# Optimization experiments

Hardware: AMD Instinct MI355X
Metric: run time of the kernel (lower is better)

The kernel has to match this reference:

```python
import jax, jax.numpy as jnp
import numpy as np

D_STATE = 16
D_CONV = 4
EXPAND = 2
GROUPS = 8
EPS = 1e-5


def _layernorm(x, w, b):
    m = x.mean(-1, keepdims=True)
    v = x.var(-1, keepdims=True)
    return (x - m) * jax.lax.rsqrt(v + EPS) * w + b


def _groupnorm(x, w, b):
    B, C = x.shape[:2]
    sp = x.shape[2:]
    xg = x.reshape(B, GROUPS, C // GROUPS, -1)
    m = xg.mean(axis=(2, 3), keepdims=True)
    v = xg.var(axis=(2, 3), keepdims=True)
    xg = (xg - m) * jax.lax.rsqrt(v + EPS)
    x = xg.reshape((B, C) + sp)
    shp = (1, C) + (1,) * len(sp)
    return x * w.reshape(shp) + b.reshape(shp)


def _mamba(xn, in_w, conv_w, conv_b, xp_w, dt_w, dt_b, A_log, Dp, out_w):
    # xn: [B, L, C]
    B, L, C = xn.shape
    di = in_w.shape[0] // 2
    rank = dt_w.shape[1]
    N = D_STATE
    xz = xn @ in_w.T                              # [B, L, 2*di]
    xi, z = xz[..., :di], xz[..., di:]
    # causal depthwise conv1d along L (pad left d_conv-1, truncate to L)
    xc = jnp.moveaxis(xi, 1, 2)                   # [B, di, L]
    xpd = jnp.pad(xc, ((0, 0), (0, 0), (D_CONV - 1, 0)))
    conv = conv_b[None, :, None]
    for k in range(D_CONV):
        conv = conv + conv_w[None, :, k, None] * xpd[:, :, k:k + L]
    u = jnp.moveaxis(jax.nn.silu(conv), 1, 2)     # [B, L, di]
    dbl = u @ xp_w.T                              # [B, L, rank+2N]
    dt = dbl[..., :rank]
    Bm = dbl[..., rank:rank + N]
    Cm = dbl[..., rank + N:]
    delta = jax.nn.softplus(dt @ dt_w.T + dt_b)   # [B, L, di]
    A = -jnp.exp(A_log)                           # [di, N]
    dA = jnp.exp(delta[..., None] * A)            # [B, L, di, N]
    dBu = delta[..., None] * Bm[:, :, None, :] * u[..., None]

    def comb(e1, e2):
        a1, b1 = e1
        a2, b2 = e2
        return a1 * a2, a2 * b1 + b2

    _, h = jax.lax.associative_scan(comb, (dA, dBu), axis=1)  # h_t = dA_t*h_{t-1} + dBu_t
    y = jnp.einsum('bldn,bln->bld', h, Cm) + u * Dp
    y = y * jax.nn.silu(z)
    return y @ out_w.T


def _mamba_layer(x, p):
    B, C = x.shape[:2]
    img = x.shape[2:]
    L = int(np.prod(img))
    xf = jnp.moveaxis(x.reshape(B, C, L), 1, 2)   # [B, L, C]
    xn = _layernorm(xf, p['ln_w'], p['ln_b'])
    xm = _mamba(xn, p['in_w'], p['conv_w'], p['conv_b'], p['xp_w'],
                p['dt_w'], p['dt_b'], p['A_log'], p['Dp'], p['out_w'])
    xm = xm + p['skip'] * xf
    xm = _layernorm(xm, p['ln_w'], p['ln_b'])     # same norm params reused, as in source
    y = xm @ p['proj_w'].T + p['proj_b']
    return jnp.moveaxis(y, 1, 2).reshape((B, C) + img)


def setup_inputs() -> dict:
    key = jax.random.key(0)
    B, C = 2, 48
    img = (16, 32, 32)
    di = EXPAND * C
    rank = -(-C // 16)
    ks = iter(jax.random.split(key, 64))

    def nrm(shape, scale):
        return jax.random.normal(next(ks), shape, jnp.float32) * scale

    inp = {'x': jax.random.normal(next(ks), (B, C) + img, jnp.float32)}
    inp['gn1_w'] = jnp.ones(C); inp['gn1_b'] = jnp.zeros(C)
    inp['gn2_w'] = jnp.ones(C); inp['gn2_b'] = jnp.zeros(C)
    for i in (1, 2):
        inp[f'ln{i}_w'] = jnp.ones(C); inp[f'ln{i}_b'] = jnp.zeros(C)
        inp[f'in_w{i}'] = nrm((2 * di, C), C ** -0.5)
        inp[f'conv_w{i}'] = nrm((di, D_CONV), D_CONV ** -0.5)
        inp[f'conv_b{i}'] = jnp.zeros(di)
        inp[f'xp_w{i}'] = nrm((rank + 2 * D_STATE, di), di ** -0.5)
        inp[f'dt_w{i}'] = nrm((di, rank), rank ** -0.5)
        inp[f'dt_b{i}'] = nrm((di,), 0.1) - 4.0  # softplus -> small positive dt
        inp[f'A_log{i}'] = jnp.log(jnp.tile(jnp.arange(1, D_STATE + 1, dtype=jnp.float32), (di, 1)))
        inp[f'D{i}'] = jnp.ones(di)
        inp[f'out_w{i}'] = nrm((C, di), di ** -0.5)
        inp[f'proj_w{i}'] = nrm((C, C), C ** -0.5)
        inp[f'proj_b{i}'] = jnp.zeros(C)
        inp[f'skip{i}'] = jnp.ones(1)
    return inp


def reference(x, gn1_w, gn1_b, gn2_w, gn2_b,
              ln1_w, ln1_b, in_w1, conv_w1, conv_b1, xp_w1, dt_w1, dt_b1, A_log1, D1, out_w1, proj_w1, proj_b1, skip1,
              ln2_w, ln2_b, in_w2, conv_w2, conv_b2, xp_w2, dt_w2, dt_b2, A_log2, D2, out_w2, proj_w2, proj_b2, skip2):
    p1 = dict(ln_w=ln1_w, ln_b=ln1_b, in_w=in_w1, conv_w=conv_w1, conv_b=conv_b1, xp_w=xp_w1,
              dt_w=dt_w1, dt_b=dt_b1, A_log=A_log1, Dp=D1, out_w=out_w1, proj_w=proj_w1,
              proj_b=proj_b1, skip=skip1)
    p2 = dict(ln_w=ln2_w, ln_b=ln2_b, in_w=in_w2, conv_w=conv_w2, conv_b=conv_b2, xp_w=xp_w2,
              dt_w=dt_w2, dt_b=dt_b2, A_log=A_log2, Dp=D2, out_w=out_w2, proj_w=proj_w2,
              proj_b=proj_b2, skip=skip2)
    identity = x
    h = jax.nn.relu(_groupnorm(x, gn1_w, gn1_b))
    h = _mamba_layer(h, p1)
    h = jax.nn.relu(_groupnorm(h, gn2_w, gn2_b))
    h = _mamba_layer(h, p2)
    return h + identity
```

## Files before the change

kernel.cpp:

```cpp
#include <hip/hip_runtime.h>
#include <hip/hip_bf16.h>

#define LCH   48
#define DI    96
#define LSEQ  16384
#define NB    2
#define NPOS  (NB*LSEQ)
#define NSTATE 16
#define CPG   6
#define EPS   1e-5f
#define NC    128
#define CL    128
#define NCHAIN (NB*DI*NSTATE)
#define TS    32
#define TSS   36

typedef __hip_bfloat16 bf16;

__device__ __forceinline__ float LDW(const void* p, size_t i, bool f32){
    return f32 ? ((const float*)p)[i] : __bfloat162float(((const bf16*)p)[i]);
}

__device__ __forceinline__ float bf2f(unsigned short h){
    union { unsigned int i; float f; } u; u.i = ((unsigned int)h) << 16; return u.f;
}

__device__ __forceinline__ float4 LDW4(const void* p, size_t i4, bool f32){
    if (f32) return ((const float4*)p)[i4];
    ushort4 v = ((const ushort4*)p)[i4];
    return make_float4(bf2f(v.x), bf2f(v.y), bf2f(v.z), bf2f(v.w));
}

__device__ __forceinline__ float row16_sum(float p){
    union { float f; int i; } u, v;
    u.f = p; v.i = __builtin_amdgcn_mov_dpp(u.i, 0x111, 0xf, 0xf, true); p += v.f;
    u.f = p; v.i = __builtin_amdgcn_mov_dpp(u.i, 0x112, 0xf, 0xf, true); p += v.f;
    u.f = p; v.i = __builtin_amdgcn_mov_dpp(u.i, 0x114, 0xf, 0xf, true); p += v.f;
    u.f = p; v.i = __builtin_amdgcn_mov_dpp(u.i, 0x118, 0xf, 0xf, true); p += v.f;
    return p;
}

__global__ void k_flag(const void* gnw, int* flag, float* __restrict__ acc1, float* __restrict__ acc2){
    int t = threadIdx.x;
    if (t == 0){
        const unsigned short* g = (const unsigned short*)gnw;
        flag[0] = (g[0] == 0x3F80) ? 0 : 1;
    }
    if (t < 32){ acc1[t] = 0.f; acc2[t] = 0.f; }
}

__global__ void k_gnpart_x(const void* __restrict__ x, const int* Fg, float* __restrict__ acc){
    const bool f32 = Fg[0];
    int bg = blockIdx.x >> 4, sl = blockIdx.x & 15;
    int b = bg >> 3, g = bg & 7;
    int tid = threadIdx.x;
    float s = 0.f, q = 0.f;
    for (int c = 0; c < CPG; ++c){
        size_t base = (size_t)(b*LCH + g*CPG + c)*LSEQ + sl*1024;
        float4 v = LDW4(x, base/4 + tid, f32);
        s += v.x; q += v.x*v.x;
        s += v.y; q += v.y*v.y;
        s += v.z; q += v.z*v.z;
        s += v.w; q += v.w*v.w;
    }
    __shared__ float ss[256], sq[256];
    ss[tid] = s; sq[tid] = q; __syncthreads();
    for (int st = 128; st > 0; st >>= 1){
        if (tid < st){ ss[tid] += ss[tid+st]; sq[tid] += sq[tid+st]; }
        __syncthreads();
    }
    if (tid == 0){
        atomicAdd(&acc[bg*2],   ss[0]);
        atomicAdd(&acc[bg*2+1], sq[0]);
    }
}

template<int SRC>
__global__ void k_prepin(const void* __restrict__ src, const int* Fg, const float* __restrict__ acc,
                         const void* gnw, const void* gnb, const void* lnw, const void* lnb,
                         const void* __restrict__ inw,
                         float* __restrict__ xf, float* __restrict__ xi, float* __restrict__ z){
    const bool f32 = Fg[0];
    __shared__ float wl[96*52];
    __shared__ float xl[32*52];
    __shared__ float fl[32*52];
    __shared__ float sst[32];
    int tid = threadIdx.x;
    int part = blockIdx.x & 1;
    int pos0 = (blockIdx.x >> 1)*32;
    int b = pos0 >> 14, l0 = pos0 & (LSEQ-1);
    if (tid < 16){
        float mean = acc[tid*2] / (float)(CPG*LSEQ);
        float var  = acc[tid*2+1] / (float)(CPG*LSEQ) - mean*mean;
        sst[tid*2]   = mean;
        sst[tid*2+1] = rsqrtf(var + EPS);
    }
    for (int i = tid; i < 96*12; i += 256){
        int o = i/12, k4 = i - o*12;
        ((float4*)wl)[o*13+k4] = LDW4(inw, (size_t)part*1152 + i, f32);
    }
    if (SRC == 0){
        for (int i = tid; i < 48*32; i += 256){
            int c = i >> 5, p = i & 31;
            xl[p*52+c] = LDW(src, (size_t)(b*LCH+c)*LSEQ + l0 + p, f32);
        }
    } else {
        const float4* ms4 = (const float4*)src;
        for (int i = tid; i < 32*12; i += 256){
            int p = i/12, c4 = i - p*12;
            ((float4*)xl)[p*13+c4] = ms4[(size_t)pos0*12 + i];
        }
    }
    __syncthreads();
    if (tid < 32){
        float* row  = xl + tid*52;
        float* frow = fl + tid*52;
        float s = 0.f, q = 0.f;
        #pragma unroll
        for (int c = 0; c < LCH; ++c){
            int g = c / CPG;
            float mean = sst[(b*8+g)*2], rs = sst[(b*8+g)*2+1];
            float v = row[c];
            v = (v - mean)*rs*LDW(gnw,c,f32) + LDW(gnb,c,f32);
            v = fmaxf(v, 0.f);
            frow[c] = v; s += v; q += v*v;
        }
        float mean = s / (float)LCH;
        float rs = rsqrtf(q/(float)LCH - mean*mean + EPS);
        #pragma unroll
        for (int c = 0; c < LCH; ++c)
            row[c] = (frow[c]-mean)*rs*LDW(lnw,c,f32) + LDW(lnb,c,f32);
    }
    __syncthreads();
    if (part == 0){
        float4* xf4 = (float4*)xf;
        const float4* fl4 = (const float4*)fl;
        for (int i = tid; i < 32*12; i += 256){
            int p = i/12, c4 = i - p*12;
            xf4[(size_t)pos0*12 + i] = fl4[p*13+c4];
        }
    }
    float* dst = part ? z : xi;
    int o  = tid & 31;
    int pg = tid >> 5;
    const float4* wl4 = (const float4*)wl;
    const float4* xl4 = (const float4*)xl;
    float a0[4] = {0.f,0.f,0.f,0.f};
    float a1[4] = {0.f,0.f,0.f,0.f};
    float a2[4] = {0.f,0.f,0.f,0.f};
    #pragma unroll
    for (int k4 = 0; k4 < 12; ++k4){
        float4 w0 = wl4[ o     *13 + k4];
        float4 w1 = wl4[(o+32)*13 + k4];
        float4 w2 = wl4[(o+64)*13 + k4];
        #pragma unroll
        for (int q = 0; q < 4; ++q){
            float4 xv = xl4[(pg*4+q)*13 + k4];
            a0[q] += xv.x*w0.x; a0[q] += xv.y*w0.y; a0[q] += xv.z*w0.z; a0[q] += xv.w*w0.w;
            a1[q] += xv.x*w1.x; a1[q] += xv.y*w1.y; a1[q] += xv.z*w1.z; a1[q] += xv.w*w1.w;
            a2[q] += xv.x*w2.x; a2[q] += xv.y*w2.y; a2[q] += xv.z*w2.z; a2[q] += xv.w*w2.w;
        }
    }
    #pragma unroll
    for (int q = 0; q < 4; ++q){
        size_t pos = (size_t)(pos0 + pg*4 + q);
        dst[pos*DI + o     ] = a0[q];
        dst[pos*DI + o + 32] = a1[q];
        dst[pos*DI + o + 64] = a2[q];
    }
}

__global__ void k_convdbl(const float* __restrict__ xi, const void* cw, const void* cb,
                          const void* __restrict__ xpw, const void* dtw, const void* dtb,
                          const int* Fg, float* __restrict__ u_g, float* __restrict__ B2,
                          float* __restrict__ C2, float* __restrict__ delta_g){
    const bool f32 = Fg[0];
    __shared__ float xil[35*100];
    __shared__ float wbc[32*100];
    __shared__ float wdt[3*100];
    __shared__ float cwl[96*4];
    __shared__ float cbl[96];
    __shared__ float dtwl[96*3];
    __shared__ float dtbl[96];
    __shared__ float dtl[32*3];
    int tid = threadIdx.x;
    int pos0 = blockIdx.x*32;
    int l0 = pos0 & (LSEQ-1);

    for (int i = tid; i < 32*24; i += 256){
        int o = i/24, k4 = i - o*24;
        int row = (o & 1) ? (19 + (o>>1)) : (3 + (o>>1));
        ((float4*)wbc)[o*25 + k4] = LDW4(xpw, (size_t)row*24 + k4, f32);
    }
    if (tid < 72){
        int o = tid/24, k4 = tid - o*24;
        ((float4*)wdt)[o*25 + k4] = LDW4(xpw, (size_t)o*24 + k4, f32);
    }
    for (int i = tid; i < 96*4; i += 256) cwl[i] = LDW(cw, i, f32);
    if (tid < 96) cbl[tid] = LDW(cb, tid, f32);
    for (int i = tid; i < 96*3; i += 256) dtwl[i] = LDW(dtw, i, f32);
    if (tid >= 128 && tid < 224) dtbl[tid-128] = LDW(dtb, tid-128, f32);
    {
        float4* xv = (float4*)xil;
        const float4* gx = (const float4*)xi;
        for (int i = tid; i < 35*24; i += 256){
            int p = i/24, k4 = i - p*24;
            float4 v = make_float4(0.f, 0.f, 0.f, 0.f);
            if (l0 + p - 3 >= 0) v = gx[(size_t)(pos0-3+p)*24 + k4];
            xv[p*25 + k4] = v;
        }
    }
    __syncthreads();

    float uu[12];
    #pragma unroll
    for (int r = 0; r < 12; ++r){
        int i = tid + 256*r;
        int j = i/96, d = i - j*96;
        float4 cw4 = ((const float4*)cwl)[d];
        float acc = cbl[d];
        acc += cw4.x*xil[(j+0)*100+d];
        acc += cw4.y*xil[(j+1)*100+d];
        acc += cw4.z*xil[(j+2)*100+d];
        acc += cw4.w*xil[(j+3)*100+d];
        uu[r] = acc / (1.f + __expf(-acc));
    }
    __syncthreads();

    #pragma unroll
    for (int r = 0; r < 12; ++r){
        int i = tid + 256*r;
        int j = i/96, d = i - j*96;
        xil[j*100+d] = uu[r];
        u_g[(size_t)pos0*DI + i] = uu[r];
    }
    __syncthreads();

    {
        int o  = tid & 31;
        int pg = ((tid>>6)<<1) | ((tid>>5)&1);
        const float4* ulv = (const float4*)xil;
        const float4* wv  = (const float4*)wbc;
        float a0=0.f, a1=0.f, a2=0.f, a3=0.f;
        #pragma unroll 4
        for (int k4 = 0; k4 < 24; ++k4){
            float4 u0 = ulv[(pg*4+0)*25 + k4];
            float4 u1 = ulv[(pg*4+1)*25 + k4];
            float4 u2 = ulv[(pg*4+2)*25 + k4];
            float4 u3 = ulv[(pg*4+3)*25 + k4];
            float4 w  = wv[o*25 + k4];
            a0 += u0.x*w.x; a0 += u0.y*w.y; a0 += u0.z*w.z; a0 += u0.w*w.w;
            a1 += u1.x*w.x; a1 += u1.y*w.y; a1 += u1.z*w.z; a1 += u1.w*w.w;
            a2 += u2.x*w.x; a2 += u2.y*w.y; a2 += u2.z*w.z; a2 += u2.w*w.w;
            a3 += u3.x*w.x; a3 += u3.y*w.y; a3 += u3.z*w.z; a3 += u3.w*w.w;
        }
        int nn = o >> 1;
        float* dst = (o & 1) ? C2 : B2;
        size_t pb = (size_t)(pos0 + pg*4);
        dst[(pb+0)*16 + nn] = a0;
        dst[(pb+1)*16 + nn] = a1;
        dst[(pb+2)*16 + nn] = a2;
        dst[(pb+3)*16 + nn] = a3;
    }
    if (tid < 96){
        int o = tid >> 5;
        int p = tid & 31;
        const float4* ulv = (const float4*)xil;
        const float4* wv  = (const float4*)wdt;
        float a = 0.f;
        #pragma unroll 4
        for (int k4 = 0; k4 < 24; ++k4){
            float4 uv = ulv[p*25 + k4];
            float4 w  = wv[o*25 + k4];
            a += uv.x*w.x; a += uv.y*w.y; a += uv.z*w.z; a += uv.w*w.w;
        }
        dtl[p*3+o] = a;
    }
    __syncthreads();

    for (int i = tid; i < 32*96; i += 256){
        int p = i/96, d = i - p*96;
        float acc = dtbl[d];
        #pragma unroll
        for (int r = 0; r < 3; ++r) acc += dtl[p*3+r]*dtwl[d*3+r];
        float sp = (acc > 20.f) ? acc : log1pf(__expf(acc));
        delta_g[(size_t)pos0*DI + i] = sp;
    }
}

__global__ void k_scanA(const float* __restrict__ delta, const float* __restrict__ u,
                        const float* __restrict__ B2, const void* Alog, const int* Fg,
                        float* __restrict__ Pb, float* __restrict__ Sb){
    const bool f32 = Fg[0];
    __shared__ float dls[2][16*TSS];
    __shared__ float uus[2][16*TSS];
    __shared__ float bbs[2][16*TSS];
    int tid = threadIdx.x;
    int t = blockIdx.x*256 + tid;
    int n = tid & 15;
    int sg0 = blockIdx.x*16;
    int cb2 = sg0/96;
    int d0 = sg0 - cb2*96;
    int b = cb2 & 1, chunk = cb2 >> 1;
    int dloc = tid >> 4;
    int d = d0 + dloc;
    float An = -__expf(LDW(Alog, d*16+n, f32));
    float P = 1.f, S = 0.f;
    int base = b*LSEQ + chunk*CL;
    int si0 = tid >> 4, sj = tid & 15;
    int si1 = si0 + 16;
    float pd0, pd1, pu0, pu1, pb0, pb1;
    auto fetch = [&](int tb){
        pd0 = delta[(size_t)(tb+si0)*DI + d0 + sj];
        pu0 = u    [(size_t)(tb+si0)*DI + d0 + sj];
        pb0 = B2   [(size_t)(tb+si0)*16 + sj];
        pd1 = delta[(size_t)(tb+si1)*DI + d0 + sj];
        pu1 = u    [(size_t)(tb+si1)*DI + d0 + sj];
        pb1 = B2   [(size_t)(tb+si1)*16 + sj];
    };
    auto store = [&](int bs){
        dls[bs][sj*TSS+si0] = pd0; dls[bs][sj*TSS+si1] = pd1;
        uus[bs][sj*TSS+si0] = pu0; uus[bs][sj*TSS+si1] = pu1;
        bbs[bs][sj*TSS+si0] = pb0; bbs[bs][sj*TSS+si1] = pb1;
    };
    fetch(base); store(0);
    __syncthreads();
    for (int tile = 0; tile < CL/TS; ++tile){
        int cur = tile & 1;
        if (tile+1 < CL/TS) fetch(base + (tile+1)*TS);
        #pragma unroll
        for (int i4 = 0; i4 < TS/4; ++i4){
            float4 dl4 = *(const float4*)&dls[cur][dloc*TSS + i4*4];
            float4 uu4 = *(const float4*)&uus[cur][dloc*TSS + i4*4];
            float4 bn4 = *(const float4*)&bbs[cur][n   *TSS + i4*4];
            float a;
            a = __expf(dl4.x*An); P *= a; S = a*S + dl4.x*bn4.x*uu4.x;
            a = __expf(dl4.y*An); P *= a; S = a*S + dl4.y*bn4.y*uu4.y;
            a = __expf(dl4.z*An); P *= a; S = a*S + dl4.z*bn4.z*uu4.z;
            a = __expf(dl4.w*An); P *= a; S = a*S + dl4.w*bn4.w*uu4.w;
        }
        if (tile+1 < CL/TS) store(1-cur);
        __syncthreads();
    }
    Pb[t] = P; Sb[t] = S;
}

__global__ void k_scanB(const float* __restrict__ Pb, const float* __restrict__ Sb,
                        float* __restrict__ carry){
    int ch = blockIdx.x*blockDim.x + threadIdx.x;
    float c = 0.f;
    for (int cb = 0; cb < NC; cb += 8){
        float P[8], S[8];
        #pragma unroll
        for (int j = 0; j < 8; ++j){
            P[j] = Pb[(size_t)(cb+j)*NCHAIN + ch];
            S[j] = Sb[(size_t)(cb+j)*NCHAIN + ch];
        }
        #pragma unroll
        for (int j = 0; j < 8; ++j){
            carry[(size_t)(cb+j)*NCHAIN + ch] = c;
            c = S[j] + P[j]*c;
        }
    }
}

__global__ void k_scanC(const float* __restrict__ delta, const float* __restrict__ u,
                        const float* __restrict__ B2, const float* __restrict__ C2,
                        const float* __restrict__ carry, const void* Alog, const void* Dp,
                        const int* Fg, float* __restrict__ y){
    const bool f32 = Fg[0];
    __shared__ float dls[2][16*TSS];
    __shared__ float uus[2][16*TSS];
    __shared__ float bbs[2][16*TSS];
    __shared__ float ccs[2][16*TSS];
    int tid = threadIdx.x;
    int n = tid & 15;
    int sg0 = blockIdx.x*16;
    int cb2 = sg0/96;
    int d0 = sg0 - cb2*96;
    int b = cb2 & 1, chunk = cb2 >> 1;
    int dloc = tid >> 4;
    int d = d0 + dloc;
    float An = -__expf(LDW(Alog, d*16+n, f32));
    float Dpd = LDW(Dp, d, f32);
    float h = carry[chunk*NCHAIN + (b*DI+d)*NSTATE + n];
    int base = b*LSEQ + chunk*CL;
    int si0 = tid >> 4, sj = tid & 15;
    int si1 = si0 + 16;
    float pd0, pd1, pu0, pu1, pb0, pb1, pc0, pc1;
    auto fetch = [&](int tb){
        pd0 = delta[(size_t)(tb+si0)*DI + d0 + sj];
        pu0 = u    [(size_t)(tb+si0)*DI + d0 + sj];
        pb0 = B2   [(size_t)(tb+si0)*16 + sj];
        pc0 = C2   [(size_t)(tb+si0)*16 + sj];
        pd1 = delta[(size_t)(tb+si1)*DI + d0 + sj];
        pu1 = u    [(size_t)(tb+si1)*DI + d0 + sj];
        pb1 = B2   [(size_t)(tb+si1)*16 + sj];
        pc1 = C2   [(size_t)(tb+si1)*16 + sj];
    };
    auto store = [&](int bs){
        dls[bs][sj*TSS+si0] = pd0; dls[bs][sj*TSS+si1] = pd1;
        uus[bs][sj*TSS+si0] = pu0; uus[bs][sj*TSS+si1] = pu1;
        bbs[bs][sj*TSS+si0] = pb0; bbs[bs][sj*TSS+si1] = pb1;
        ccs[bs][sj*TSS+si0] = pc0; ccs[bs][sj*TSS+si1] = pc1;
    };
    fetch(base); store(0);
    __syncthreads();
    for (int tile = 0; tile < CL/TS; ++tile){
        int cur = tile & 1;
        int tb = base + tile*TS;
        if (tile+1 < CL/TS) fetch(base + (tile+1)*TS);
        #pragma unroll
        for (int i4 = 0; i4 < TS/4; ++i4){
            float4 dl4 = *(const float4*)&dls[cur][dloc*TSS + i4*4];
            float4 uu4 = *(const float4*)&uus[cur][dloc*TSS + i4*4];
            float4 bn4 = *(const float4*)&bbs[cur][n   *TSS + i4*4];
            float4 cn4 = *(const float4*)&ccs[cur][n   *TSS + i4*4];
            float a, p;
            a = __expf(dl4.x*An); h = a*h + dl4.x*bn4.x*uu4.x;
            p = row16_sum(h*cn4.x);
            if (n == 15) y[(size_t)(tb+i4*4+0)*DI + d] = p + uu4.x*Dpd;
            a = __expf(dl4.y*An); h = a*h + dl4.y*bn4.y*uu4.y;
            p = row16_sum(h*cn4.y);
            if (n == 15) y[(size_t)(tb+i4*4+1)*DI + d] = p + uu4.y*Dpd;
            a = __expf(dl4.z*An); h = a*h + dl4.z*bn4.z*uu4.z;
            p = row16_sum(h*cn4.z);
            if (n == 15) y[(size_t)(tb+i4*4+2)*DI + d] = p + uu4.z*Dpd;
            a = __expf(dl4.w*An); h = a*h + dl4.w*bn4.w*uu4.w;
            p = row16_sum(h*cn4.w);
            if (n == 15) y[(size_t)(tb+i4*4+3)*DI + d] = p + uu4.w*Dpd;
        }
        if (tile+1 < CL/TS) store(1-cur);
        __syncthreads();
    }
}

__global__ void k_outproj(const float* __restrict__ psum, const void* __restrict__ outw,
                          const void* skipv, const int* Fg,
                          const float* __restrict__ zx,
                          const float* __restrict__ xf, float* __restrict__ xm){
    const bool f32 = Fg[0];
    __shared__ float wl[48*100];
    __shared__ float yl[32*100];
    int tid = threadIdx.x;
    int pos0 = blockIdx.x*32;
    for (int i = tid; i < 48*24; i += 256){
        int o = i/24, k4 = i - o*24;
        ((float4*)wl)[o*25+k4] = LDW4(outw, i, f32);
    }
    {
        const float4* ps4 = (const float4*)psum;
        const float4* zz4 = (const float4*)zx;
        for (int i = tid; i < 32*24; i += 256){
            int p = i/24, k4 = i - p*24;
            float4 pv = ps4[(size_t)pos0*24 + i];
            float4 zv = zz4[(size_t)pos0*24 + i];
            float4 y;
            y.x = pv.x * (zv.x / (1.f + __expf(-zv.x)));
            y.y = pv.y * (zv.y / (1.f + __expf(-zv.y)));
            y.z = pv.z * (zv.z / (1.f + __expf(-zv.z)));
            y.w = pv.w * (zv.w / (1.f + __expf(-zv.w)));
            ((float4*)yl)[p*25+k4] = y;
        }
    }
    __syncthreads();
    float sk = LDW(skipv, 0, f32);
    int o16 = tid & 15;
    int pg  = tid >> 4;
    const float4* wl4 = (const float4*)wl;
    const float4* yl4 = (const float4*)yl;
    float a[3][2] = {{0.f,0.f},{0.f,0.f},{0.f,0.f}};
    #pragma unroll 4
    for (int k4 = 0; k4 < 24; ++k4){
        float4 w0 = wl4[ o16     *25+k4];
        float4 w1 = wl4[(o16+16)*25+k4];
        float4 w2 = wl4[(o16+32)*25+k4];
        float4 y0 = yl4[(pg*2+0)*25+k4];
        float4 y1 = yl4[(pg*2+1)*25+k4];
        a[0][0] += y0.x*w0.x; a[0][0] += y0.y*w0.y; a[0][0] += y0.z*w0.z; a[0][0] += y0.w*w0.w;
        a[0][1] += y1.x*w0.x; a[0][1] += y1.y*w0.y; a[0][1] += y1.z*w0.z; a[0][1] += y1.w*w0.w;
        a[1][0] += y0.x*w1.x; a[1][0] += y0.y*w1.y; a[1][0] += y0.z*w1.z; a[1][0] += y0.w*w1.w;
        a[1][1] += y1.x*w1.x; a[1][1] += y1.y*w1.y; a[1][1] += y1.z*w1.z; a[1][1] += y1.w*w1.w;
        a[2][0] += y0.x*w2.x; a[2][0] += y0.y*w2.y; a[2][0] += y0.z*w2.z; a[2][0] += y0.w*w2.w;
        a[2][1] += y1.x*w2.x; a[2][1] += y1.y*w2.y; a[2][1] += y1.z*w2.z; a[2][1] += y1.w*w2.w;
    }
    #pragma unroll
    for (int r = 0; r < 3; ++r){
        #pragma unroll
        for (int q = 0; q < 2; ++q){
            size_t oi = (size_t)(pos0+pg*2+q)*LCH + o16 + r*16;
            xm[oi] = a[r][q] + sk*xf[oi];
        }
    }
}

template<int FIN>
__global__ void k_lnproj(const float* __restrict__ xm, const void* lnw, const void* lnb,
                         const void* __restrict__ pw, const void* pb, const int* Fg,
                         const void* __restrict__ xres, float* __restrict__ mout,
                         float* __restrict__ acc2, void* __restrict__ outp){
    const bool f32 = Fg[0];
    __shared__ float wp[48*52];
    __shared__ float xl[32*52];
    __shared__ float ol[32*49];
    __shared__ float gs[48], gq[48];
    int tid = threadIdx.x;
    int pos0 = blockIdx.x*32;
    if (FIN == 0 && tid < 48){ gs[tid] = 0.f; gq[tid] = 0.f; }
    for (int i = tid; i < 48*12; i += 256){
        int o = i/12, k4 = i - o*12;
        ((float4*)wp)[o*13+k4] = LDW4(pw, i, f32);
    }
    {
        const float4* xm4 = (const float4*)xm;
        for (int i = tid; i < 32*12; i += 256){
            int p = i/12, c4 = i - p*12;
            ((float4*)xl)[p*13+c4] = xm4[(size_t)pos0*12 + i];
        }
    }
    __syncthreads();
    if (tid < 32){
        float* row = xl + tid*52;
        float s = 0.f, q = 0.f;
        #pragma unroll
        for (int c = 0; c < LCH; ++c){ float v = row[c]; s += v; q += v*v; }
        float mean = s / (float)LCH;
        float rs = rsqrtf(q/(float)LCH - mean*mean + EPS);
        #pragma unroll
        for (int c = 0; c < LCH; ++c)
            row[c] = (row[c]-mean)*rs*LDW(lnw,c,f32) + LDW(lnb,c,f32);
    }
    __syncthreads();
    int o16 = tid & 15;
    int pg  = tid >> 4;
    float b0 = LDW(pb, o16,      f32);
    float b1 = LDW(pb, o16 + 16, f32);
    float b2 = LDW(pb, o16 + 32, f32);
    const float4* wp4 = (const float4*)wp;
    const float4* xl4 = (const float4*)xl;
    float a[3][2] = {{b0,b0},{b1,b1},{b2,b2}};
    #pragma unroll 4
    for (int k4 = 0; k4 < 12; ++k4){
        float4 w0 = wp4[ o16     *13+k4];
        float4 w1 = wp4[(o16+16)*13+k4];
        float4 w2 = wp4[(o16+32)*13+k4];
        float4 x0 = xl4[(pg*2+0)*13+k4];
        float4 x1 = xl4[(pg*2+1)*13+k4];
        a[0][0] += x0.x*w0.x; a[0][0] += x0.y*w0.y; a[0][0] += x0.z*w0.z; a[0][0] += x0.w*w0.w;
        a[0][1] += x1.x*w0.x; a[0][1] += x1.y*w0.y; a[0][1] += x1.z*w0.z; a[0][1] += x1.w*w0.w;
        a[1][0] += x0.x*w1.x; a[1][0] += x0.y*w1.y; a[1][0] += x0.z*w1.z; a[1][0] += x0.w*w1.w;
        a[1][1] += x1.x*w1.x; a[1][1] += x1.y*w1.y; a[1][1] += x1.z*w1.z; a[1][1] += x1.w*w1.w;
        a[2][0] += x0.x*w2.x; a[2][0] += x0.y*w2.y; a[2][0] += x0.z*w2.z; a[2][0] += x0.w*w2.w;
        a[2][1] += x1.x*w2.x; a[2][1] += x1.y*w2.y; a[2][1] += x1.z*w2.z; a[2][1] += x1.w*w2.w;
    }
    if (FIN == 0){
        float sl[3] = {0.f,0.f,0.f}, ql[3] = {0.f,0.f,0.f};
        #pragma unroll
        for (int r = 0; r < 3; ++r){
            #pragma unroll
            for (int q = 0; q < 2; ++q){
                float v = a[r][q];
                mout[(size_t)(pos0+pg*2+q)*LCH + o16 + r*16] = v;
                sl[r] += v; ql[r] += v*v;
            }
        }
        #pragma unroll
        for (int r = 0; r < 3; ++r){
            atomicAdd(&gs[o16 + r*16], sl[r]);
            atomicAdd(&gq[o16 + r*16], ql[r]);
        }
        __syncthreads();
        if (tid < 8){
            int b = pos0 >> 14;
            float s = 0.f, q = 0.f;
            #pragma unroll
            for (int c = 0; c < CPG; ++c){ s += gs[tid*CPG+c]; q += gq[tid*CPG+c]; }
            atomicAdd(&acc2[(b*8+tid)*2],   s);
            atomicAdd(&acc2[(b*8+tid)*2+1], q);
        }
    } else {
        #pragma unroll
        for (int r = 0; r < 3; ++r){
            #pragma unroll
            for (int q = 0; q < 2; ++q)
                ol[(pg*2+q)*49 + o16 + r*16] = a[r][q];
        }
        __syncthreads();
        int b = pos0 >> 14, l0 = pos0 & (LSEQ-1);
        for (int i = tid; i < 48*32; i += 256){
            int c = i >> 5, p = i & 31;
            size_t gi = (size_t)(b*LCH+c)*LSEQ + l0 + p;
            float v = ol[p*49+c] + LDW(xres, gi, f32);
            if (f32) ((float*)outp)[gi] = v;
            else     ((bf16*)outp)[gi] = __float2bfloat16(v);
        }
    }
}

extern "C" void kernel_launch(void* const* d_in, const int* in_sizes, int n_in,
                              void* d_out, int out_size, void* d_ws, size_t ws_size,
                              hipStream_t stream){
    const void* x = d_in[0];
    auto W = [&](int i){ return (const void*)d_in[i]; };

    float* ws = (float*)d_ws;
    size_t off = 0;
    int*   flag  = (int*)ws;  off += 16;
    float* acc1  = ws + off;  off += 32;
    float* acc2  = ws + off;  off += 32;
    float* xf    = ws + off;  off += (size_t)NPOS*LCH;
    float* xi    = ws + off;  off += (size_t)NPOS*DI;
    float* zb    = ws + off;  off += (size_t)NPOS*DI;
    float* ub    = ws + off;  off += (size_t)NPOS*DI;
    float* B2    = ws + off;  off += (size_t)NPOS*16;
    float* C2    = ws + off;  off += (size_t)NPOS*16;
    float* Pb    = ws + off;  off += (size_t)NC*NCHAIN;
    float* Sb    = ws + off;  off += (size_t)NC*NCHAIN;
    float* carry = ws + off;  off += (size_t)NC*NCHAIN;
    float* delta = ws + off;  off += (size_t)NPOS*DI;
    float* mbuf  = ws + off;  off += (size_t)NPOS*LCH;
    float* ybuf  = xi;
    float* xmbuf = delta;

    k_flag<<<1, 64, 0, stream>>>(W(1), flag, acc1, acc2);

    k_gnpart_x<<<256, 256, 0, stream>>>(x, flag, acc1);
    k_prepin<0><<<2*NPOS/32, 256, 0, stream>>>(x, flag, acc1, W(1), W(2), W(5), W(6), W(7), xf, xi, zb);
    k_convdbl<<<NPOS/32, 256, 0, stream>>>(xi, W(8), W(9), W(10), W(11), W(12), flag, ub, B2, C2, delta);
    k_scanA<<<NC*NCHAIN/256, 256, 0, stream>>>(delta, ub, B2, W(13), flag, Pb, Sb);
    k_scanB<<<NCHAIN/256, 256, 0, stream>>>(Pb, Sb, carry);
    k_scanC<<<NC*NCHAIN/256, 256, 0, stream>>>(delta, ub, B2, C2, carry, W(13), W(14), flag, ybuf);
    k_outproj<<<NPOS/32, 256, 0, stream>>>(ybuf, W(15), W(18), flag, zb, xf, xmbuf);
    k_lnproj<0><<<NPOS/32, 256, 0, stream>>>(xmbuf, W(5), W(6), W(16), W(17), flag, nullptr, mbuf, acc2, nullptr);

    k_prepin<1><<<2*NPOS/32, 256, 0, stream>>>(mbuf, flag, acc2, W(3), W(4), W(19), W(20), W(21), xf, xi, zb);
    k_convdbl<<<NPOS/32, 256, 0, stream>>>(xi, W(22), W(23), W(24), W(25), W(26), flag, ub, B2, C2, delta);
    k_scanA<<<NC*NCHAIN/256, 256, 0, stream>>>(delta, ub, B2, W(27), flag, Pb, Sb);
    k_scanB<<<NCHAIN/256, 256, 0, stream>>>(Pb, Sb, carry);
    k_scanC<<<NC*NCHAIN/256, 256, 0, stream>>>(delta, ub, B2, C2, carry, W(27), W(28), flag, ybuf);
    k_outproj<<<NPOS/32, 256, 0, stream>>>(ybuf, W(29), W(32), flag, zb, xf, xmbuf);
    k_lnproj<1><<<NPOS/32, 256, 0, stream>>>(xmbuf, W(19), W(20), W(30), W(31), flag, x, nullptr, nullptr, d_out);
}
```

Baseline: 433.1 us.

## Parallelize row norms across 8 lanes, halve scan chunk length, use exp2

The per-row group-norm and layer-norm passes now split each 48-channel row across 8 threads, each handling 6 channels, and reduce with wave shuffles instead of one thread looping over all 48. The scan chunk length drops from 128 to 64 and the chunk count doubles, which shortens the serial work per scan block at the cost of a longer carry pass. The exponentials in the scan use exp2 with log2(e) folded into A. Group-stat shared atomics are first reduced across lanes with shuffles so fewer atomics are issued.

```diff
diff --git a/kernel.cpp b/kernel.cpp
--- a/kernel.cpp
+++ b/kernel.cpp
@@ -9,11 +9,12 @@
 #define NSTATE 16
 #define CPG   6
 #define EPS   1e-5f
-#define NC    128
-#define CL    128
+#define NC    256
+#define CL    64
 #define NCHAIN (NB*DI*NSTATE)
 #define TS    32
 #define TSS   36
+#define LOG2E 1.442695040888963f
 
 typedef __hip_bfloat16 bf16;
 
@@ -112,24 +113,31 @@
         }
     }
     __syncthreads();
-    if (tid < 32){
-        float* row  = xl + tid*52;
-        float* frow = fl + tid*52;
-        float s = 0.f, q = 0.f;
-        #pragma unroll
-        for (int c = 0; c < LCH; ++c){
-            int g = c / CPG;
-            float mean = sst[(b*8+g)*2], rs = sst[(b*8+g)*2+1];
-            float v = row[c];
-            v = (v - mean)*rs*LDW(gnw,c,f32) + LDW(gnb,c,f32);
+    {
+        int row = tid >> 3, q = tid & 7;
+        float* rrow = xl + row*52;
+        float* frow = fl + row*52;
+        float gmean = sst[(b*8+q)*2], grs = sst[(b*8+q)*2+1];
+        float vv[6];
+        float s = 0.f, qq = 0.f;
+        #pragma unroll
+        for (int j = 0; j < 6; ++j){
+            int c = q*6 + j;
+            float v = rrow[c];
+            v = (v - gmean)*grs*LDW(gnw,c,f32) + LDW(gnb,c,f32);
             v = fmaxf(v, 0.f);
-            frow[c] = v; s += v; q += v*v;
-        }
+            vv[j] = v; frow[c] = v; s += v; qq += v*v;
+        }
+        s  += __shfl_xor(s, 1);  qq += __shfl_xor(qq, 1);
+        s  += __shfl_xor(s, 2);  qq += __shfl_xor(qq, 2);
+        s  += __shfl_xor(s, 4);  qq += __shfl_xor(qq, 4);
         float mean = s / (float)LCH;
-        float rs = rsqrtf(q/(float)LCH - mean*mean + EPS);
-        #pragma unroll
-        for (int c = 0; c < LCH; ++c)
-            row[c] = (frow[c]-mean)*rs*LDW(lnw,c,f32) + LDW(lnb,c,f32);
+        float rs = rsqrtf(qq/(float)LCH - mean*mean + EPS);
+        #pragma unroll
+        for (int j = 0; j < 6; ++j){
+            int c = q*6 + j;
+            rrow[c] = (vv[j]-mean)*rs*LDW(lnw,c,f32) + LDW(lnb,c,f32);
+        }
     }
     __syncthreads();
     if (part == 0){
@@ -304,7 +312,7 @@
     int b = cb2 & 1, chunk = cb2 >> 1;
     int dloc = tid >> 4;
     int d = d0 + dloc;
-    float An = -__expf(LDW(Alog, d*16+n, f32));
+    float An = -__expf(LDW(Alog, d*16+n, f32)) * LOG2E;
     float P = 1.f, S = 0.f;
     int base = b*LSEQ + chunk*CL;
     int si0 = tid >> 4, sj = tid & 15;
@@ -334,10 +342,10 @@
             float4 uu4 = *(const float4*)&uus[cur][dloc*TSS + i4*4];
             float4 bn4 = *(const float4*)&bbs[cur][n   *TSS + i4*4];
             float a;
-            a = __expf(dl4.x*An); P *= a; S = a*S + dl4.x*bn4.x*uu4.x;
-            a = __expf(dl4.y*An); P *= a; S = a*S + dl4.y*bn4.y*uu4.y;
-            a = __expf(dl4.z*An); P *= a; S = a*S + dl4.z*bn4.z*uu4.z;
-            a = __expf(dl4.w*An); P *= a; S = a*S + dl4.w*bn4.w*uu4.w;
+            a = exp2f(dl4.x*An); P *= a; S = a*S + dl4.x*bn4.x*uu4.x;
+            a = exp2f(dl4.y*An); P *= a; S = a*S + dl4.y*bn4.y*uu4.y;
+            a = exp2f(dl4.z*An); P *= a; S = a*S + dl4.z*bn4.z*uu4.z;
+            a = exp2f(dl4.w*An); P *= a; S = a*S + dl4.w*bn4.w*uu4.w;
         }
         if (tile+1 < CL/TS) store(1-cur);
         __syncthreads();
@@ -381,7 +389,7 @@
     int b = cb2 & 1, chunk = cb2 >> 1;
     int dloc = tid >> 4;
     int d = d0 + dloc;
-    float An = -__expf(LDW(Alog, d*16+n, f32));
+    float An = -__expf(LDW(Alog, d*16+n, f32)) * LOG2E;
     float Dpd = LDW(Dp, d, f32);
     float h = carry[chunk*NCHAIN + (b*DI+d)*NSTATE + n];
     int base = b*LSEQ + chunk*CL;
@@ -417,16 +425,16 @@
             float4 bn4 = *(const float4*)&bbs[cur][n   *TSS + i4*4];
             float4 cn4 = *(const float4*)&ccs[cur][n   *TSS + i4*4];
             float a, p;
-            a = __expf(dl4.x*An); h = a*h + dl4.x*bn4.x*uu4.x;
+            a = exp2f(dl4.x*An); h = a*h + dl4.x*bn4.x*uu4.x;
             p = row16_sum(h*cn4.x);
             if (n == 15) y[(size_t)(tb+i4*4+0)*DI + d] = p + uu4.x*Dpd;
-            a = __expf(dl4.y*An); h = a*h + dl4.y*bn4.y*uu4.y;
+            a = exp2f(dl4.y*An); h = a*h + dl4.y*bn4.y*uu4.y;
             p = row16_sum(h*cn4.y);
             if (n == 15) y[(size_t)(tb+i4*4+1)*DI + d] = p + uu4.y*Dpd;
-            a = __expf(dl4.z*An); h = a*h + dl4.z*bn4.z*uu4.z;
+            a = exp2f(dl4.z*An); h = a*h + dl4.z*bn4.z*uu4.z;
             p = row16_sum(h*cn4.z);
             if (n == 15) y[(size_t)(tb+i4*4+2)*DI + d] = p + uu4.z*Dpd;
-            a = __expf(dl4.w*An); h = a*h + dl4.w*bn4.w*uu4.w;
+            a = exp2f(dl4.w*An); h = a*h + dl4.w*bn4.w*uu4.w;
             p = row16_sum(h*cn4.w);
             if (n == 15) y[(size_t)(tb+i4*4+3)*DI + d] = p + uu4.w*Dpd;
         }
@@ -519,16 +527,26 @@
         }
     }
     __syncthreads();
-    if (tid < 32){
-        float* row = xl + tid*52;
-        float s = 0.f, q = 0.f;
-        #pragma unroll
-        for (int c = 0; c < LCH; ++c){ float v = row[c]; s += v; q += v*v; }
+    {
+        int row = tid >> 3, q = tid & 7;
+        float* rrow = xl + row*52;
+        float vv[6];
+        float s = 0.f, qq = 0.f;
+        #pragma unroll
+        for (int j = 0; j < 6; ++j){
+            float v = rrow[q*6+j];
+            vv[j] = v; s += v; qq += v*v;
+        }
+        s  += __shfl_xor(s, 1);  qq += __shfl_xor(qq, 1);
+        s  += __shfl_xor(s, 2);  qq += __shfl_xor(qq, 2);
+        s  += __shfl_xor(s, 4);  qq += __shfl_xor(qq, 4);
         float mean = s / (float)LCH;
-        float rs = rsqrtf(q/(float)LCH - mean*mean + EPS);
-        #pragma unroll
-        for (int c = 0; c < LCH; ++c)
-            row[c] = (row[c]-mean)*rs*LDW(lnw,c,f32) + LDW(lnb,c,f32);
+        float rs = rsqrtf(qq/(float)LCH - mean*mean + EPS);
+        #pragma unroll
+        for (int j = 0; j < 6; ++j){
+            int c = q*6 + j;
+            rrow[c] = (vv[j]-mean)*rs*LDW(lnw,c,f32) + LDW(lnb,c,f32);
+        }
     }
     __syncthreads();
     int o16 = tid & 15;
@@ -566,8 +584,13 @@
         }
         #pragma unroll
         for (int r = 0; r < 3; ++r){
-            atomicAdd(&gs[o16 + r*16], sl[r]);
-            atomicAdd(&gq[o16 + r*16], ql[r]);
+            float s = sl[r], q2 = ql[r];
+            s  += __shfl_xor(s, 16);  q2 += __shfl_xor(q2, 16);
+            s  += __shfl_xor(s, 32);  q2 += __shfl_xor(q2, 32);
+            if ((tid & 63) < 16){
+                atomicAdd(&gs[o16 + r*16], s);
+                atomicAdd(&gq[o16 + r*16], q2);
+            }
         }
         __syncthreads();
         if (tid < 8){
```

Result: slower. 561.9 us (+29.8%).
